# Optimization experiments

Hardware: AMD Instinct MI355X
Metric: run time of the kernel (lower is better)

## Reference

```python
import jax, jax.numpy as jnp
import numpy as np


def setup_inputs() -> dict:
    key = jax.random.key(0)
    ks = jax.random.split(key, 8)
    B, T, H, Hu = 128, 64, 1024, 512
    MJW = 64                    # max_jump_width
    J = 2 * MJW + 1             # size_jump_width_set_nn = 129
    N = 2 * T                   # HMM states (word states + null states)
    I = 64                      # source sentence length
    sc = 0.02
    return {
        "y_hidden": jax.random.normal(ks[0], (B, T, H), jnp.float32),
        # emission probs p(source word i | state s), strictly positive for log
        "emission": jax.random.uniform(ks[1], (B, N, I), jnp.float32, 1e-4, 1.0),
        "source_lengths": jax.random.randint(ks[2], (B,), 1, I + 1),
        "W1": jax.random.normal(ks[3], (H, Hu), jnp.float32) * sc,
        "b1": jnp.zeros((Hu,), jnp.float32),
        "W2": jax.random.normal(ks[4], (Hu, J), jnp.float32) * sc,
        "b2": jnp.zeros((J,), jnp.float32),
        "W3": jax.random.normal(ks[5], (Hu, 1), jnp.float32) * sc,
        "b3": jnp.zeros((1,), jnp.float32),
        "max_jump_width": MJW,
    }


def _build_transition(y_hidden, W1, b1, W2, b2, W3, b3, mjw):
    # Dense(tanh) -> Dense softmax jump-width distribution + Dense sigmoid p0
    B, T, _ = y_hidden.shape
    ts = jnp.tanh(y_hidden @ W1 + b1)                       # [B,T,Hu]
    jw = jax.nn.softmax(ts @ W2 + b2, axis=-1)              # [B,T,J]
    p0 = jax.nn.sigmoid(jnp.squeeze(ts @ W3 + b3, -1))      # [B,T]
    r = jnp.arange(T)
    # banded gather: transition[i, j] = jw[i, mjw + j - i]
    band_idx = mjw + r[None, :] - r[:, None]                # [T,T], in [0, J)
    band = jnp.take_along_axis(jw, band_idx[None], axis=2)  # [B,T,T]
    diag_p0 = jnp.eye(T, dtype=jw.dtype) * p0[:, :, None]   # [B,T,T]
    top = jnp.concatenate([band, diag_p0], axis=2)          # [B,T,2T]
    return jnp.concatenate([top, top], axis=1)              # [B,2T,2T]


def _forward_alignment(transition, emission, source_lengths):
    # Faithful translation of the tf.scan forward algorithm. tf.scan with no
    # initializer uses elems[0] as the initial accumulator and emits it as
    # output[0] (log part = ones, so the [0,0] element is 1.0).
    B, N, I = emission.shape
    em = jnp.transpose(emission, (2, 0, 1))                 # [I,B,N]
    alpha0 = jnp.broadcast_to(em[0][:, None, :], (B, N, N)) # rows all equal e_0
    L0 = jnp.ones((B,), emission.dtype)

    def step(carry, e):
        alpha, L = carry                                    # [B,N,N], [B]
        yi = e[:, None, :]                                  # rows of yi_prob identical
        m1 = jnp.matmul(alpha, transition)                  # [B,N,N]
        tmp = m1 * yi
        tmp = tmp / jnp.sum(tmp, axis=2, keepdims=True)     # row-normalized alpha
        m2 = jnp.matmul(transition, alpha) * yi             # [B,N,N]
        max_j = jnp.max(m2, axis=-1)[:, 0]                  # gather row 0 -> [B]
        state_prev = jnp.sum(m1, axis=1)                    # [B,N]
        state = jnp.log(e) + jnp.log(state_prev) - max_j[:, None]
        state_log = jnp.log(jnp.sum(jnp.exp(state), axis=-1))
        L_new = L + state_log + max_j                       # [B]
        return (tmp, L_new), L_new

    (_, _), logs = jax.lax.scan(step, (alpha0, L0), em[1:])  # [I-1,B]
    logs = jnp.concatenate([L0[None], logs], axis=0).T       # [B,I]
    idx = (source_lengths - 1)[:, None]
    return jnp.take_along_axis(logs, idx, axis=1)[:, 0]      # [B]


def reference(y_hidden, emission, source_lengths, W1, b1, W2, b2, W3, b3, max_jump_width):
    transition = _build_transition(y_hidden, W1, b1, W2, b2, W3, b3, max_jump_width)
    return _forward_alignment(transition, emission, source_lengths)
```

## Files before the change

### kernel.cpp

```cpp
#include <hip/hip_runtime.h>
#include <hip/hip_bf16.h>

typedef float f32x4 __attribute__((ext_vector_type(4)));
typedef __bf16 bf16x8 __attribute__((ext_vector_type(8)));
typedef unsigned short u16;

#define OFF_W1T  0u
#define OFF_W23B 1048576u
#define OFF_TS   1196032u
#define OFF_JWT  9584640u
#define OFF_P0   11681792u

static __device__ __forceinline__ u16 f2bf(float x) {
    __bf16 h = (__bf16)x;
    return __builtin_bit_cast(u16, h);
}

__device__ __forceinline__ void gload16(const void* g, void* l) {
    __builtin_amdgcn_global_load_lds(
        (const __attribute__((address_space(1))) void*)g,
        (__attribute__((address_space(3))) void*)l,
        16, 0, 0);
}

__global__ __launch_bounds__(256) void prep_kernel(
    const float* __restrict__ W1, const float* __restrict__ W2,
    const float* __restrict__ W3,
    __bf16* __restrict__ W1T, __bf16* __restrict__ W23B)
{
    const int t = threadIdx.x;
    if (blockIdx.x < 128) {
        __shared__ __bf16 lds_t[64][72];
        const int kt = blockIdx.x >> 3, nt = blockIdx.x & 7;
        const int k0 = kt * 64, n0 = nt * 64;
        {
            const int kr = t >> 2, c0 = (t & 3) * 16;
            const float* src = W1 + (size_t)(k0 + kr) * 512 + n0 + c0;
            #pragma unroll
            for (int q = 0; q < 4; ++q) {
                float4 v = *(const float4*)(src + q * 4);
                lds_t[kr][c0 + q * 4 + 0] = (__bf16)v.x;
                lds_t[kr][c0 + q * 4 + 1] = (__bf16)v.y;
                lds_t[kr][c0 + q * 4 + 2] = (__bf16)v.z;
                lds_t[kr][c0 + q * 4 + 3] = (__bf16)v.w;
            }
        }
        __syncthreads();
        {
            const int nr = t >> 2, kc = (t & 3) * 16;
            bf16x8 o0, o1;
            #pragma unroll
            for (int j = 0; j < 8; ++j) o0[j] = lds_t[kc + j][nr];
            #pragma unroll
            for (int j = 0; j < 8; ++j) o1[j] = lds_t[kc + 8 + j][nr];
            __bf16* dst = W1T + (size_t)(n0 + nr) * 1024 + k0 + kc;
            *(bf16x8*)(dst)     = o0;
            *(bf16x8*)(dst + 8) = o1;
        }
    } else {
        int g = (blockIdx.x - 128) * 256 + t;
        if (g < 9216) {
            int n = g >> 6;
            int k8 = (g & 63) * 8;
            bf16x8 v;
            #pragma unroll
            for (int j = 0; j < 8; ++j) {
                int k = k8 + j;
                float x = 0.0f;
                if (n < 129) x = W2[(size_t)k * 129 + n];
                else if (n == 129) x = W3[k];
                v[j] = (__bf16)x;
            }
            int kk = k8 >> 5, lg = (k8 >> 3) & 3, ct = n >> 4, lr = n & 15;
            *(bf16x8*)&W23B[(((size_t)(kk * 9 + ct)) * 64 + lg * 16 + lr) * 8] = v;
        }
    }
}

__global__ __launch_bounds__(256, 2) void gemm1_kernel(
    const float* __restrict__ Y, const __bf16* __restrict__ W1T,
    const float* __restrict__ b1, u16* __restrict__ ts)
{
    __shared__ float  As[3][64 * 32];
    __shared__ __bf16 Bs[3][128 * 32];
    const int tid = threadIdx.x;
    const int m0 = blockIdx.x * 64, n0 = blockIdx.y * 128;
    const int wid = tid >> 6, lane = tid & 63;
    const int wr = wid >> 1, wc = wid & 1;
    const int lr = lane & 15, lg = lane >> 4;

    const int al = lane >> 3;
    const int au = (lane & 7) ^ al;
    const float* yA0 = Y + (size_t)(m0 + (wid * 2 + 0) * 8 + al) * 1024 + au * 4;
    const float* yA1 = Y + (size_t)(m0 + (wid * 2 + 1) * 8 + al) * 1024 + au * 4;
    const int bl = lane >> 2;
    const int bu = (lane & 3) ^ (bl & 3);
    const __bf16* wB0 = W1T + (size_t)(n0 + (wid * 2 + 0) * 16 + bl) * 1024 + bu * 8;
    const __bf16* wB1 = W1T + (size_t)(n0 + (wid * 2 + 1) * 16 + bl) * 1024 + bu * 8;

    f32x4 acc[2][4];
    #pragma unroll
    for (int m = 0; m < 2; m++)
        #pragma unroll
        for (int n = 0; n < 4; n++) { f32x4 z = {0.f,0.f,0.f,0.f}; acc[m][n] = z; }

#define STAGE(buf, kt) do { \
    gload16(yA0 + (kt) * 32, &As[buf][(wid * 2 + 0) * 256]); \
    gload16(yA1 + (kt) * 32, &As[buf][(wid * 2 + 1) * 256]); \
    gload16(wB0 + (kt) * 32, &Bs[buf][(wid * 2 + 0) * 512]); \
    gload16(wB1 + (kt) * 32, &Bs[buf][(wid * 2 + 1) * 512]); \
} while (0)

#define COMPUTE(buf) do { \
    bf16x8 af[2]; bf16x8 bfr[4]; \
    _Pragma("unroll") \
    for (int m = 0; m < 2; ++m) { \
        const int row = wr * 32 + m * 16 + lr; \
        const int r7 = row & 7; \
        float4 h0 = *(const float4*)&As[buf][row * 32 + (((lg * 2 + 0) ^ r7) * 4)]; \
        float4 h1 = *(const float4*)&As[buf][row * 32 + (((lg * 2 + 1) ^ r7) * 4)]; \
        bf16x8 tt; \
        tt[0]=(__bf16)h0.x; tt[1]=(__bf16)h0.y; tt[2]=(__bf16)h0.z; tt[3]=(__bf16)h0.w; \
        tt[4]=(__bf16)h1.x; tt[5]=(__bf16)h1.y; tt[6]=(__bf16)h1.z; tt[7]=(__bf16)h1.w; \
        af[m] = tt; \
    } \
    _Pragma("unroll") \
    for (int n = 0; n < 4; ++n) { \
        const int rowb = wc * 64 + n * 16 + lr; \
        bfr[n] = *(const bf16x8*)&Bs[buf][rowb * 32 + ((lg ^ (rowb & 3)) * 8)]; \
    } \
    __builtin_amdgcn_s_setprio(1); \
    _Pragma("unroll") \
    for (int m = 0; m < 2; ++m) \
        _Pragma("unroll") \
        for (int n = 0; n < 4; ++n) \
            acc[m][n] = __builtin_amdgcn_mfma_f32_16x16x32_bf16(af[m], bfr[n], acc[m][n], 0, 0, 0); \
    __builtin_amdgcn_s_setprio(0); \
} while (0)

#define KSTEP(buf, kt, VM, DO_STAGE) do { \
    asm volatile("s_waitcnt vmcnt(" #VM ")" ::: "memory"); \
    __builtin_amdgcn_s_barrier(); \
    COMPUTE(buf); \
    asm volatile("s_waitcnt lgkmcnt(0)" ::: "memory"); \
    __builtin_amdgcn_s_barrier(); \
    if (DO_STAGE) STAGE(buf, (kt) + 3); \
} while (0)

    STAGE(0, 0); STAGE(1, 1); STAGE(2, 2);
    #pragma unroll 1
    for (int base = 0; base < 27; base += 3) {
        KSTEP(0, base + 0, 8, 1);
        KSTEP(1, base + 1, 8, 1);
        KSTEP(2, base + 2, 8, 1);
    }
    KSTEP(0, 27, 8, 1);
    KSTEP(1, 28, 8, 1);
    KSTEP(2, 29, 8, 0);
    KSTEP(0, 30, 4, 0);
    KSTEP(1, 31, 0, 0);

    #pragma unroll
    for (int m = 0; m < 2; m++) {
        #pragma unroll
        for (int n = 0; n < 4; n++) {
            int col = n0 + wc * 64 + n * 16 + lr;
            float bias = b1[col];
            #pragma unroll
            for (int j = 0; j < 4; j++) {
                int row = m0 + wr * 32 + m * 16 + lg * 4 + j;
                float v = tanhf(acc[m][n][j] + bias);
                ts[(size_t)row * 512 + col] = f2bf(v);
            }
        }
    }
#undef STAGE
#undef COMPUTE
#undef KSTEP
}

__global__ __launch_bounds__(256) void band_kernel(
    const u16* __restrict__ ts, const u16* __restrict__ W23B,
    const float* __restrict__ b2, const float* __restrict__ b3,
    float* __restrict__ jwT, float* __restrict__ p0)
{
    const int b = blockIdx.x;
    const int tid = threadIdx.x;
    const int w = tid >> 6, lane = tid & 63;
    const int lr = lane & 15, lg = lane >> 4;
    const int r0 = b * 64 + w * 16;

    f32x4 acc[9];
    #pragma unroll
    for (int ct = 0; ct < 9; ct++) { f32x4 z = {0.f,0.f,0.f,0.f}; acc[ct] = z; }

    #pragma unroll 4
    for (int kk = 0; kk < 16; ++kk) {
        bf16x8 a = *(const bf16x8*)(ts + (size_t)(r0 + lr) * 512 + kk * 32 + lg * 8);
        #pragma unroll
        for (int ct = 0; ct < 9; ct++) {
            bf16x8 bv = *(const bf16x8*)(W23B + ((size_t)(kk * 9 + ct) * 64 + lane) * 8);
            acc[ct] = __builtin_amdgcn_mfma_f32_16x16x32_bf16(a, bv, acc[ct], 0, 0, 0);
        }
    }

    float b3v = b3[0];
    #pragma unroll
    for (int j = 0; j < 4; j++) {
        int rloc = w * 16 + lg * 4 + j;
        float v[9];
        float mx = -1e30f;
        #pragma unroll
        for (int ct = 0; ct < 9; ct++) {
            int col = ct * 16 + lr;
            if (col < 129) { float x = acc[ct][j] + b2[col]; v[ct] = x; mx = fmaxf(mx, x); }
            else v[ct] = -1e30f;
        }
        #pragma unroll
        for (int o = 1; o < 16; o <<= 1) mx = fmaxf(mx, __shfl_xor(mx, o));
        float sum = 0.f;
        #pragma unroll
        for (int ct = 0; ct < 9; ct++) {
            int col = ct * 16 + lr;
            if (col < 129) { float e = expf(v[ct] - mx); v[ct] = e; sum += e; }
        }
        #pragma unroll
        for (int o = 1; o < 16; o <<= 1) sum += __shfl_xor(sum, o);
        float inv = 1.0f / sum;
        #pragma unroll
        for (int ct = 0; ct < 9; ct++) {
            int col = ct * 16 + lr;
            int cc = col - 64 + rloc;
            if (col < 129 && cc >= 0 && cc < 64)
                jwT[((size_t)b * 64 + cc) * 64 + rloc] = v[ct] * inv;
        }
        if (lr == 1) {
            float pv = acc[8][j] + b3v;
            p0[b * 64 + rloc] = 1.0f / (1.0f + expf(-pv));
        }
    }
}

__global__ __launch_bounds__(64, 1) void recur_kernel(
    const float* __restrict__ jwT, const float* __restrict__ p0g,
    const float* __restrict__ em, const int* __restrict__ slen,
    float* __restrict__ out)
{
    __shared__ float em_s[128][65];
    __shared__ f32x4 a_bc4[16];
    const int b = blockIdx.x, c = threadIdx.x;

    const float* bb = jwT + ((size_t)b * 64 + c) * 64;
    f32x4 B0  = *(const f32x4*)(bb + 0);
    f32x4 B1  = *(const f32x4*)(bb + 4);
    f32x4 B2  = *(const f32x4*)(bb + 8);
    f32x4 B3  = *(const f32x4*)(bb + 12);
    f32x4 B4  = *(const f32x4*)(bb + 16);
    f32x4 B5  = *(const f32x4*)(bb + 20);
    f32x4 B6  = *(const f32x4*)(bb + 24);
    f32x4 B7  = *(const f32x4*)(bb + 28);
    f32x4 B8  = *(const f32x4*)(bb + 32);
    f32x4 B9  = *(const f32x4*)(bb + 36);
    f32x4 B10 = *(const f32x4*)(bb + 40);
    f32x4 B11 = *(const f32x4*)(bb + 44);
    f32x4 B12 = *(const f32x4*)(bb + 48);
    f32x4 B13 = *(const f32x4*)(bb + 52);
    f32x4 B14 = *(const f32x4*)(bb + 56);
    f32x4 B15 = *(const f32x4*)(bb + 60);

    {
        const float4* eg = (const float4*)(em + (size_t)b * 8192);
        #pragma unroll 8
        for (int q = 0; q < 32; ++q) {
            int i4 = c + q * 64;
            float4 v = eg[i4];
            int base = i4 * 4; int n = base >> 6; int ii = base & 63;
            em_s[n][ii] = v.x; em_s[n][ii + 1] = v.y; em_s[n][ii + 2] = v.z; em_s[n][ii + 3] = v.w;
        }
    }
    const float p0r = p0g[b * 64 + c];
    const int idx = slen[b] - 1;
    __syncthreads();

    float ut = em_s[c][0] + em_s[c + 64][0];
    int Eacc = 0;

    unsigned rbase = (unsigned)(uintptr_t)(__attribute__((address_space(3))) void*)&a_bc4[0];
    unsigned waddr = rbase + (unsigned)c * 4u;

    #pragma unroll 1
    for (int i = 1; i <= idx; ++i) {
        float aloc = ut;
        f32x4 A0,A1,A2,A3,A4,A5,A6,A7,A8,A9,A10,A11,A12,A13,A14,A15;
        asm volatile(
            "ds_write_b32 %17, %16\n\t"
            "s_waitcnt lgkmcnt(0)\n\t"
            "ds_read_b128 %0, %18 offset:0\n\t"
            "ds_read_b128 %1, %18 offset:16\n\t"
            "ds_read_b128 %2, %18 offset:32\n\t"
            "ds_read_b128 %3, %18 offset:48\n\t"
            "ds_read_b128 %4, %18 offset:64\n\t"
            "ds_read_b128 %5, %18 offset:80\n\t"
            "ds_read_b128 %6, %18 offset:96\n\t"
            "ds_read_b128 %7, %18 offset:112\n\t"
            "ds_read_b128 %8, %18 offset:128\n\t"
            "ds_read_b128 %9, %18 offset:144\n\t"
            "ds_read_b128 %10, %18 offset:160\n\t"
            "ds_read_b128 %11, %18 offset:176\n\t"
            "ds_read_b128 %12, %18 offset:192\n\t"
            "ds_read_b128 %13, %18 offset:208\n\t"
            "ds_read_b128 %14, %18 offset:224\n\t"
            "ds_read_b128 %15, %18 offset:240\n\t"
            "s_waitcnt lgkmcnt(0)"
            : "=&v"(A0), "=&v"(A1), "=&v"(A2),  "=&v"(A3),
              "=&v"(A4), "=&v"(A5), "=&v"(A6),  "=&v"(A7),
              "=&v"(A8), "=&v"(A9), "=&v"(A10), "=&v"(A11),
              "=&v"(A12),"=&v"(A13),"=&v"(A14), "=&v"(A15)
            : "v"(ut), "v"(waddr), "v"(rbase)
            : "memory");
        float s0 = 0.f, s1 = 0.f, s2 = 0.f, s3 = 0.f;
#define ACC4(AV, BV) do { \
        s0 = fmaf((AV)[0], (BV)[0], s0); \
        s1 = fmaf((AV)[1], (BV)[1], s1); \
        s2 = fmaf((AV)[2], (BV)[2], s2); \
        s3 = fmaf((AV)[3], (BV)[3], s3); \
} while (0)
        ACC4(A0, B0);   ACC4(A1, B1);   ACC4(A2, B2);   ACC4(A3, B3);
        ACC4(A4, B4);   ACC4(A5, B5);   ACC4(A6, B6);   ACC4(A7, B7);
        ACC4(A8, B8);   ACC4(A9, B9);   ACC4(A10, B10); ACC4(A11, B11);
        ACC4(A12, B12); ACC4(A13, B13); ACC4(A14, B14); ACC4(A15, B15);
#undef ACC4
        ut = ((s0 + s1) + (s2 + s3)) * em_s[c][i] + aloc * p0r * em_s[c + 64][i];
        int bits = __builtin_amdgcn_readfirstlane(__float_as_int(ut));
        int ef = (bits >> 23) & 255;
        Eacc += ef - 127;
        ut *= __int_as_float((254 - ef) << 23);
    }
    float r = ut;
    #pragma unroll
    for (int o = 1; o < 64; o <<= 1) r += __shfl_xor(r, o);
    if (c == 0) {
        float res = 1.0f;
        if (idx > 0)
            res = 1.0f + 0.6931471805599453f * ((float)Eacc + __log2f(r) + 7.0f * (float)idx);
        out[b] = res;
    }
}

extern "C" void kernel_launch(void* const* d_in, const int* in_sizes, int n_in,
                              void* d_out, int out_size, void* d_ws, size_t ws_size,
                              hipStream_t stream)
{
    const float* Y   = (const float*)d_in[0];
    const float* em  = (const float*)d_in[1];
    const int*   sl  = (const int*)d_in[2];
    const float* W1  = (const float*)d_in[3];
    const float* b1  = (const float*)d_in[4];
    const float* W2  = (const float*)d_in[5];
    const float* b2  = (const float*)d_in[6];
    const float* W3  = (const float*)d_in[7];
    const float* b3  = (const float*)d_in[8];
    float* out = (float*)d_out;
    char* ws = (char*)d_ws;

    __bf16* W1T  = (__bf16*)(ws + OFF_W1T);
    __bf16* W23B = (__bf16*)(ws + OFF_W23B);
    u16*    ts   = (u16*)(ws + OFF_TS);
    float*  jwT  = (float*)(ws + OFF_JWT);
    float*  p0   = (float*)(ws + OFF_P0);

    prep_kernel<<<164, 256, 0, stream>>>(W1, W2, W3, W1T, W23B);
    dim3 g1(128, 4);
    gemm1_kernel<<<g1, 256, 0, stream>>>(Y, W1T, b1, ts);
    band_kernel<<<128, 256, 0, stream>>>(ts, (const u16*)W23B, b2, b3, jwT, p0);
    recur_kernel<<<128, 64, 0, stream>>>(jwT, p0, em, sl, out);
}
```

Before: 85.07 us.

## Deepen GEMM1 staging to four buffers and trim waits in forward recursion

```diff
diff --git a/kernel.cpp b/kernel.cpp
--- a/kernel.cpp
+++ b/kernel.cpp
@@ -81,8 +81,8 @@
     const float* __restrict__ Y, const __bf16* __restrict__ W1T,
     const float* __restrict__ b1, u16* __restrict__ ts)
 {
-    __shared__ float  As[3][64 * 32];
-    __shared__ __bf16 Bs[3][128 * 32];
+    __shared__ float  As[4][64 * 32];
+    __shared__ __bf16 Bs[4][128 * 32];
     const int tid = threadIdx.x;
     const int m0 = blockIdx.x * 64, n0 = blockIdx.y * 128;
     const int wid = tid >> 6, lane = tid & 63;
@@ -94,7 +94,7 @@
     const float* yA0 = Y + (size_t)(m0 + (wid * 2 + 0) * 8 + al) * 1024 + au * 4;
     const float* yA1 = Y + (size_t)(m0 + (wid * 2 + 1) * 8 + al) * 1024 + au * 4;
     const int bl = lane >> 2;
-    const int bu = (lane & 3) ^ (bl & 3);
+    const int bu = (lane & 3) ^ ((bl >> 1) & 3);
     const __bf16* wB0 = W1T + (size_t)(n0 + (wid * 2 + 0) * 16 + bl) * 1024 + bu * 8;
     const __bf16* wB1 = W1T + (size_t)(n0 + (wid * 2 + 1) * 16 + bl) * 1024 + bu * 8;
 
@@ -127,7 +127,7 @@
     _Pragma("unroll") \
     for (int n = 0; n < 4; ++n) { \
         const int rowb = wc * 64 + n * 16 + lr; \
-        bfr[n] = *(const bf16x8*)&Bs[buf][rowb * 32 + ((lg ^ (rowb & 3)) * 8)]; \
+        bfr[n] = *(const bf16x8*)&Bs[buf][rowb * 32 + ((lg ^ ((rowb >> 1) & 3)) * 8)]; \
     } \
     __builtin_amdgcn_s_setprio(1); \
     _Pragma("unroll") \
@@ -142,23 +142,22 @@
     asm volatile("s_waitcnt vmcnt(" #VM ")" ::: "memory"); \
     __builtin_amdgcn_s_barrier(); \
     COMPUTE(buf); \
-    asm volatile("s_waitcnt lgkmcnt(0)" ::: "memory"); \
-    __builtin_amdgcn_s_barrier(); \
-    if (DO_STAGE) STAGE(buf, (kt) + 3); \
+    if (DO_STAGE) STAGE(((kt) + 3) & 3, (kt) + 3); \
 } while (0)
 
     STAGE(0, 0); STAGE(1, 1); STAGE(2, 2);
     #pragma unroll 1
-    for (int base = 0; base < 27; base += 3) {
+    for (int base = 0; base < 28; base += 4) {
         KSTEP(0, base + 0, 8, 1);
         KSTEP(1, base + 1, 8, 1);
         KSTEP(2, base + 2, 8, 1);
-    }
-    KSTEP(0, 27, 8, 1);
-    KSTEP(1, 28, 8, 1);
-    KSTEP(2, 29, 8, 0);
-    KSTEP(0, 30, 4, 0);
-    KSTEP(1, 31, 0, 0);
+        KSTEP(3, base + 3, 8, 1);
+    }
+    KSTEP(0, 28, 8, 0);
+    STAGE(3, 31);
+    KSTEP(1, 29, 8, 0);
+    KSTEP(2, 30, 4, 0);
+    KSTEP(3, 31, 0, 0);
 
     #pragma unroll
     for (int m = 0; m < 2; m++) {
@@ -288,13 +287,15 @@
     unsigned rbase = (unsigned)(uintptr_t)(__attribute__((address_space(3))) void*)&a_bc4[0];
     unsigned waddr = rbase + (unsigned)c * 4u;
 
+    float em_lo = em_s[c][1];
+    float em_hi = em_s[c + 64][1];
+
     #pragma unroll 1
     for (int i = 1; i <= idx; ++i) {
         float aloc = ut;
         f32x4 A0,A1,A2,A3,A4,A5,A6,A7,A8,A9,A10,A11,A12,A13,A14,A15;
         asm volatile(
             "ds_write_b32 %17, %16\n\t"
-            "s_waitcnt lgkmcnt(0)\n\t"
             "ds_read_b128 %0, %18 offset:0\n\t"
             "ds_read_b128 %1, %18 offset:16\n\t"
             "ds_read_b128 %2, %18 offset:32\n\t"
@@ -318,23 +319,32 @@
               "=&v"(A12),"=&v"(A13),"=&v"(A14), "=&v"(A15)
             : "v"(ut), "v"(waddr), "v"(rbase)
             : "memory");
+        float nlo = em_s[c][i + 1];
+        float nhi = em_s[c + 64][i + 1];
         float s0 = 0.f, s1 = 0.f, s2 = 0.f, s3 = 0.f;
-#define ACC4(AV, BV) do { \
+        float s4 = 0.f, s5 = 0.f, s6 = 0.f, s7 = 0.f;
+#define ACC8(AV, BV, CV, DV) do { \
         s0 = fmaf((AV)[0], (BV)[0], s0); \
         s1 = fmaf((AV)[1], (BV)[1], s1); \
         s2 = fmaf((AV)[2], (BV)[2], s2); \
         s3 = fmaf((AV)[3], (BV)[3], s3); \
+        s4 = fmaf((CV)[0], (DV)[0], s4); \
+        s5 = fmaf((CV)[1], (DV)[1], s5); \
+        s6 = fmaf((CV)[2], (DV)[2], s6); \
+        s7 = fmaf((CV)[3], (DV)[3], s7); \
 } while (0)
-        ACC4(A0, B0);   ACC4(A1, B1);   ACC4(A2, B2);   ACC4(A3, B3);
-        ACC4(A4, B4);   ACC4(A5, B5);   ACC4(A6, B6);   ACC4(A7, B7);
-        ACC4(A8, B8);   ACC4(A9, B9);   ACC4(A10, B10); ACC4(A11, B11);
-        ACC4(A12, B12); ACC4(A13, B13); ACC4(A14, B14); ACC4(A15, B15);
-#undef ACC4
-        ut = ((s0 + s1) + (s2 + s3)) * em_s[c][i] + aloc * p0r * em_s[c + 64][i];
+        ACC8(A0, B0,  A1, B1);   ACC8(A2, B2,  A3, B3);
+        ACC8(A4, B4,  A5, B5);   ACC8(A6, B6,  A7, B7);
+        ACC8(A8, B8,  A9, B9);   ACC8(A10, B10, A11, B11);
+        ACC8(A12, B12, A13, B13); ACC8(A14, B14, A15, B15);
+#undef ACC8
+        float sum = ((s0 + s1) + (s2 + s3)) + ((s4 + s5) + (s6 + s7));
+        ut = sum * em_lo + aloc * p0r * em_hi;
         int bits = __builtin_amdgcn_readfirstlane(__float_as_int(ut));
         int ef = (bits >> 23) & 255;
         Eacc += ef - 127;
         ut *= __int_as_float((254 - ef) << 23);
+        em_lo = nlo; em_hi = nhi;
     }
     float r = ut;
     #pragma unroll
```

New measurement: 79.98 us. -6.0%, faster.
